# Optimization experiments

Measured on AMD Instinct MI355X. Metric: run time of the kernel, lower is better.

The kernel has to match this reference:

```python
import jax, jax.numpy as jnp
import numpy as np


def setup_inputs() -> dict:
    key = jax.random.key(0)
    ks = jax.random.split(key, 8)
    N, E, H, C, L, G = 100000, 1600000, 128, 10, 5, 64
    x = jax.random.normal(ks[0], (N, H), dtype=jnp.float32)
    edge_index = jax.random.randint(ks[1], (2, E), 0, N, dtype=jnp.int32)
    batch = jnp.sort(jax.random.randint(ks[2], (N,), 0, G, dtype=jnp.int32))
    # Glorot-ish init scale for stability
    Ws = jax.random.normal(ks[3], (L, H, H), dtype=jnp.float32) * (1.0 / np.sqrt(H))
    bs = jax.random.normal(ks[4], (L, H), dtype=jnp.float32) * 0.01
    W_out = jax.random.normal(ks[5], (H, C), dtype=jnp.float32) * (1.0 / np.sqrt(H))
    b_out = jax.random.normal(ks[6], (C,), dtype=jnp.float32) * 0.01
    return {"x": x, "edge_index": edge_index, "batch": batch, "num_graphs": G,
            "Ws": Ws, "bs": bs, "W_out": W_out, "b_out": b_out}


def reference(x, edge_index, batch, num_graphs, Ws, bs, W_out, b_out):
    N = x.shape[0]
    # --- GCN normalization (add self-loops, symmetric deg^-1/2 norm), computed once ---
    loop = jnp.arange(N, dtype=edge_index.dtype)
    src = jnp.concatenate([edge_index[0], loop])  # message sources (x_j)
    dst = jnp.concatenate([edge_index[1], loop])  # aggregation targets
    deg = jax.ops.segment_sum(jnp.ones_like(dst, dtype=x.dtype), dst, num_segments=N)
    dis = jnp.where(deg > 0, jax.lax.rsqrt(jnp.maximum(deg, 1.0)), 0.0)
    norm = dis[src] * dis[dst]  # [E+N]
    # --- stacked GCNConv + ReLU ---
    for l in range(Ws.shape[0]):
        xw = x @ Ws[l]                                   # [N, H] dense transform
        msg = norm[:, None] * xw[src]                    # gather + scale per edge
        x = jax.nn.relu(jax.ops.segment_sum(msg, dst, num_segments=N) + bs[l])
    # --- global mean pool over graphs ---
    sums = jax.ops.segment_sum(x, batch, num_segments=num_graphs)       # [G, H]
    cnts = jax.ops.segment_sum(jnp.ones((N,), x.dtype), batch, num_segments=num_graphs)
    pooled = sums / jnp.maximum(cnts, 1.0)[:, None]
    return pooled @ W_out + b_out
```

## Files before the change

kernel.cpp:

```cpp
#include <hip/hip_runtime.h>
#include <hip/hip_bf16.h>
#include <stdint.h>

#define HDIM 128

typedef __attribute__((ext_vector_type(8))) short short8;
typedef __attribute__((ext_vector_type(4))) float f32x4;

__device__ __forceinline__ ushort f2bf(float f) {
  uint u = __float_as_uint(f);
  u = (u + 0x7fffu + ((u >> 16) & 1u)) >> 16;
  return (ushort)u;
}
__device__ __forceinline__ float bflo(uint v) { return __uint_as_float(v << 16); }
__device__ __forceinline__ float bfhi(uint v) { return __uint_as_float(v & 0xffff0000u); }


__global__ __launch_bounds__(256) void count_kernel(const int* __restrict__ ei,
                                                    int* __restrict__ cnt, int E) {
  int i = blockIdx.x * 256 + threadIdx.x;
  if (i < E) atomicAdd(&cnt[ei[E + i]], 1);
}

__global__ __launch_bounds__(256) void dis_kernel(const int* __restrict__ cnt,
                                                  float* __restrict__ dis, int N) {
  int i = blockIdx.x * 256 + threadIdx.x;
  if (i < N) dis[i] = rsqrtf((float)(cnt[i] + 1));
}

__device__ __forceinline__ int pdeg4(int c) { return (c + 4) & ~3; }

__global__ __launch_bounds__(256) void scan1(const int* __restrict__ cnt,
                                             int* __restrict__ bsum, int N) {
  __shared__ int red[256];
  int b = blockIdx.x, t = threadIdx.x;
  int base = b * 1024;
  int s = 0;
  for (int i = t; i < 1024; i += 256) {
    int n = base + i;
    if (n < N) s += pdeg4(cnt[n]);
  }
  red[t] = s;
  __syncthreads();
  for (int off = 128; off; off >>= 1) {
    if (t < off) red[t] += red[t + off];
    __syncthreads();
  }
  if (t == 0) bsum[b] = red[0];
}

__global__ __launch_bounds__(256) void scan2(int* __restrict__ bsum, int nb) {
  __shared__ int sh[256];
  int t = threadIdx.x;
  int v = (t < nb) ? bsum[t] : 0;
  sh[t] = v;
  __syncthreads();
  for (int off = 1; off < 256; off <<= 1) {
    int add = (t >= off) ? sh[t - off] : 0;
    __syncthreads();
    sh[t] += add;
    __syncthreads();
  }
  if (t < nb) bsum[t] = sh[t] - v;
}

__global__ __launch_bounds__(256) void scan3(const int* __restrict__ cnt,
                                             const int* __restrict__ bsum,
                                             int* __restrict__ rowptr,
                                             int* __restrict__ cursor, int N) {
  __shared__ int sh[256];
  int b = blockIdx.x, t = threadIdx.x;
  int base = b * 1024 + t * 4;
  int v[4];
#pragma unroll
  for (int i = 0; i < 4; ++i) {
    int n = base + i;
    v[i] = (n < N) ? pdeg4(cnt[n]) : 0;
  }
  int tsum = v[0] + v[1] + v[2] + v[3];
  sh[t] = tsum;
  __syncthreads();
  for (int off = 1; off < 256; off <<= 1) {
    int add = (t >= off) ? sh[t - off] : 0;
    __syncthreads();
    sh[t] += add;
    __syncthreads();
  }
  int p = sh[t] - tsum + bsum[b];
#pragma unroll
  for (int i = 0; i < 4; ++i) {
    int n = base + i;
    if (n <= N) rowptr[n] = p;
    if (n < N) cursor[n] = p;
    p += v[i];
  }
}

__device__ __forceinline__ uint pack_cw(int src, float w) {
  uint w15 = (__float_as_uint(w) + 0x8000u) >> 16;
  return (uint)src | (w15 << 17);
}
__device__ __forceinline__ uint cw_src(uint u) { return u & 0x1FFFFu; }
__device__ __forceinline__ float cw_w(uint u) { return __uint_as_float((u >> 17) << 16); }

__global__ __launch_bounds__(256) void fill_csr(const int* __restrict__ ei,
                                                const float* __restrict__ dis,
                                                int* __restrict__ cursor,
                                                uint* __restrict__ colw, int E, int N) {
  int i = blockIdx.x * 256 + threadIdx.x;
  if (i < E) {
    int s = ei[i], d = ei[E + i];
    int pos = atomicAdd(&cursor[d], 1);
    colw[pos] = pack_cw(s, dis[s] * dis[d]);
  } else if (i < E + N) {
    int n = i - E;
    int pos = atomicAdd(&cursor[n], 1);
    colw[pos] = pack_cw(n, dis[n] * dis[n]);
  }
}

__global__ __launch_bounds__(256) void pad_csr(const int* __restrict__ cnt,
                                               const int* __restrict__ rowptr,
                                               uint* __restrict__ colw, int N) {
  int n = blockIdx.x * 256 + threadIdx.x;
  if (n >= N) return;
  int beg = rowptr[n] + cnt[n] + 1, end = rowptr[n + 1];
  for (int j = beg; j < end; ++j) colw[j] = (uint)n;
}

__global__ __launch_bounds__(256) void swz_w(const float* __restrict__ Ws,
                                             ushort* __restrict__ Wsw, int total) {
  int idx = blockIdx.x * 256 + threadIdx.x;
  if (idx >= total) return;
  int l = idx >> 14, r = idx & 16383;
  int j = r & 7, lane = (r >> 3) & 63, kk = (r >> 9) & 3, c = r >> 11;
  int n = c * 16 + (lane & 15);
  int k = kk * 32 + (lane >> 4) * 8 + j;
  Wsw[idx] = f2bf(Ws[l * 16384 + k * HDIM + n]);
}


template <bool F32IN>
__global__ __launch_bounds__(256) void gemm_kernel(const void* __restrict__ Xin,
                                                   const ushort* __restrict__ Wsw,
                                                   ushort* __restrict__ XW, int N,
                                                   int ntiles) {
  __shared__ ushort wlds[16384];
  __shared__ ushort clds[64 * 136];
  const int t = threadIdx.x;
  {
    const int4* src = (const int4*)Wsw;
    int4* dst = (int4*)wlds;
#pragma unroll
    for (int i = 0; i < 8; ++i) dst[t + 256 * i] = src[t + 256 * i];
  }
  __syncthreads();

  const int wave = t >> 6, lane = t & 63;
  const int kq = lane >> 4;

  for (int tile = blockIdx.x; tile < ntiles; tile += gridDim.x) {
    const int row0 = tile * 64 + wave * 16 + (lane & 15);
    const bool inb = row0 < N;

    short8 afr[4];
#pragma unroll
    for (int kk = 0; kk < 4; ++kk) afr[kk] = short8{0, 0, 0, 0, 0, 0, 0, 0};
    if (inb) {
      if constexpr (F32IN) {
        const float* arow = (const float*)Xin + (size_t)row0 * HDIM;
#pragma unroll
        for (int kk = 0; kk < 4; ++kk) {
          float4 x0 = *(const float4*)(arow + kk * 32 + kq * 8);
          float4 x1 = *(const float4*)(arow + kk * 32 + kq * 8 + 4);
          short8 f;
          f[0] = (short)f2bf(x0.x); f[1] = (short)f2bf(x0.y);
          f[2] = (short)f2bf(x0.z); f[3] = (short)f2bf(x0.w);
          f[4] = (short)f2bf(x1.x); f[5] = (short)f2bf(x1.y);
          f[6] = (short)f2bf(x1.z); f[7] = (short)f2bf(x1.w);
          afr[kk] = f;
        }
      } else {
        const short8* arow = (const short8*)((const ushort*)Xin + (size_t)row0 * HDIM);
#pragma unroll
        for (int kk = 0; kk < 4; ++kk) afr[kk] = arow[kk * 4 + kq];
      }
    }

    f32x4 acc[8];
#pragma unroll
    for (int c = 0; c < 8; ++c) acc[c] = f32x4{0.f, 0.f, 0.f, 0.f};
#pragma unroll
    for (int kk = 0; kk < 4; ++kk) {
#pragma unroll
      for (int c = 0; c < 8; ++c) {
        short8 bfr = *(const short8*)(wlds + (((c * 4 + kk) * 64 + lane) << 3));
        acc[c] = __builtin_amdgcn_mfma_f32_16x16x32_bf16(afr[kk], bfr, acc[c], 0, 0, 0);
      }
    }

    __syncthreads();
    const int m0 = wave * 16 + kq * 4;
#pragma unroll
    for (int c = 0; c < 8; ++c) {
      int col = c * 16 + (lane & 15);
#pragma unroll
      for (int r = 0; r < 4; ++r) clds[(m0 + r) * 136 + col] = f2bf(acc[c][r]);
    }
    __syncthreads();
#pragma unroll
    for (int i = 0; i < 4; ++i) {
      int idx = t + 256 * i;
      int row = idx >> 4, piece = idx & 15;
      int grow = tile * 64 + row;
      if (grow < N)
        ((int4*)XW)[(size_t)tile * 1024 + idx] =
            *(const int4*)(clds + row * 136 + piece * 8);
    }
  }
}

__global__ __launch_bounds__(256, 6) void agg_kernel(const ushort* __restrict__ XW,
                                                     const uint* __restrict__ colw,
                                                     const int* __restrict__ rowptr,
                                                     const float* __restrict__ bias,
                                                     ushort* __restrict__ Y, int N) {
  const int lane = threadIdx.x & 63;
  const int node = blockIdx.x * 4 + (threadIdx.x >> 6);
  if (node >= N) return;
  const int e = lane >> 4, c = lane & 15;
  const int beg = rowptr[node];
  const int pdeg = rowptr[node + 1] - beg;
  const int last = pdeg - 1;

  uint cw[6];
#pragma unroll
  for (int k = 0; k < 6; ++k) {
    int off = 4 * k + e;
    cw[k] = __builtin_nontemporal_load(colw + beg + (off < pdeg ? off : last));
  }
  uint4 gv[6];
#pragma unroll
  for (int k = 0; k < 6; ++k)
    gv[k] = *(const uint4*)(XW + ((size_t)cw_src(cw[k]) << 7) + c * 8);

  float acc[8];
#pragma unroll
  for (int i = 0; i < 8; ++i) acc[i] = 0.f;

#pragma unroll
  for (int k = 0; k < 6; ++k) {
    int off = 4 * k + e;
    float w = (off < pdeg) ? cw_w(cw[k]) : 0.f;
    uint4 v = gv[k];
    acc[0] += w * bflo(v.x); acc[1] += w * bfhi(v.x);
    acc[2] += w * bflo(v.y); acc[3] += w * bfhi(v.y);
    acc[4] += w * bflo(v.z); acc[5] += w * bfhi(v.z);
    acc[6] += w * bflo(v.w); acc[7] += w * bfhi(v.w);
  }
  for (int off = 24 + e; off < pdeg; off += 4) {
    uint u = __builtin_nontemporal_load(colw + beg + off);
    uint4 v = *(const uint4*)(XW + ((size_t)cw_src(u) << 7) + c * 8);
    float w = cw_w(u);
    acc[0] += w * bflo(v.x); acc[1] += w * bfhi(v.x);
    acc[2] += w * bflo(v.y); acc[3] += w * bfhi(v.y);
    acc[4] += w * bflo(v.z); acc[5] += w * bfhi(v.z);
    acc[6] += w * bflo(v.w); acc[7] += w * bfhi(v.w);
  }

#pragma unroll
  for (int i = 0; i < 8; ++i) {
    acc[i] += __shfl_xor(acc[i], 16, 64);
    acc[i] += __shfl_xor(acc[i], 32, 64);
  }
  if (e == 0) {
    float4 b0 = *(const float4*)(bias + c * 8);
    float4 b1 = *(const float4*)(bias + c * 8 + 4);
    uint4 pk;
    pk.x = (uint)f2bf(fmaxf(acc[0] + b0.x, 0.f)) | ((uint)f2bf(fmaxf(acc[1] + b0.y, 0.f)) << 16);
    pk.y = (uint)f2bf(fmaxf(acc[2] + b0.z, 0.f)) | ((uint)f2bf(fmaxf(acc[3] + b0.w, 0.f)) << 16);
    pk.z = (uint)f2bf(fmaxf(acc[4] + b1.x, 0.f)) | ((uint)f2bf(fmaxf(acc[5] + b1.y, 0.f)) << 16);
    pk.w = (uint)f2bf(fmaxf(acc[6] + b1.z, 0.f)) | ((uint)f2bf(fmaxf(acc[7] + b1.w, 0.f)) << 16);
    *(uint4*)(Y + (size_t)node * HDIM + c * 8) = pk;
  }
}


__global__ __launch_bounds__(256) void pool_partial(const ushort* __restrict__ x,
                                                    const int* __restrict__ batch,
                                                    float* __restrict__ pooled,
                                                    int* __restrict__ gcnt, int N) {
  const int g = blockIdx.x, s = blockIdx.y;
  const int t = threadIdx.x;
  __shared__ int range[2];
  __shared__ float sums[256];
  if (t < 2) {
    int target = g + t;
    int lo = 0, hi = N;
    while (lo < hi) {
      int mid = (lo + hi) >> 1;
      if (batch[mid] < target) lo = mid + 1;
      else hi = mid;
    }
    range[t] = lo;
  }
  __syncthreads();
  int beg = range[0], end = range[1];
  if (s == 0 && t == 0) gcnt[g] = end - beg;
  int col = t & 127, half = t >> 7;
  float acc = 0.f;
  for (int n = beg + s * 2 + half; n < end; n += 16) {
    acc += __uint_as_float(((uint)x[(size_t)n * HDIM + col]) << 16);
  }
  sums[t] = acc;
  __syncthreads();
  if (t < 128) atomicAdd(&pooled[g * HDIM + t], sums[t] + sums[t + 128]);
}

__global__ __launch_bounds__(256) void out_final(const float* __restrict__ pooled,
                                                 const int* __restrict__ gcnt,
                                                 const float* __restrict__ W_out,
                                                 const float* __restrict__ b_out,
                                                 float* __restrict__ out, int G, int C) {
  int i = blockIdx.x * 256 + threadIdx.x;
  if (i >= G * C) return;
  int g = i / C, c = i - g * C;
  float inv = 1.f / (float)max(gcnt[g], 1);
  const float* pg = pooled + g * HDIM;
  float o = 0.f;
  for (int h = 0; h < HDIM; ++h) o += pg[h] * W_out[h * C + c];
  out[i] = b_out[c] + o * inv;
}


extern "C" void kernel_launch(void* const* d_in, const int* in_sizes, int n_in,
                              void* d_out, int out_size, void* d_ws, size_t ws_size,
                              hipStream_t stream) {
  (void)n_in;
  (void)ws_size;
  const float* x = (const float*)d_in[0];
  const int* ei = (const int*)d_in[1];
  const int* batch = (const int*)d_in[2];
  const float* Ws = (const float*)d_in[4];
  const float* bs = (const float*)d_in[5];
  const float* W_out = (const float*)d_in[6];
  const float* b_out = (const float*)d_in[7];
  float* out = (float*)d_out;

  const int N = in_sizes[0] / HDIM;
  const int E = in_sizes[1] / 2;
  const int L = in_sizes[5] / HDIM;
  const int C = in_sizes[7];
  const int G = out_size / C;

  char* p = (char*)d_ws;
  auto carve = [&](size_t bytes) {
    char* r = p;
    p += (bytes + 255) & ~(size_t)255;
    return r;
  };
  int* cnt = (int*)carve((size_t)N * 4);
  float* dis = (float*)carve((size_t)N * 4);
  int* rowptr = (int*)carve((size_t)(N + 1) * 4);
  int* cursor = (int*)carve((size_t)N * 4);
  int* bsum = (int*)carve(4096);
  uint* colw = (uint*)carve(((size_t)E + 4 * (size_t)N + 64) * 4);
  ushort* Wsw = (ushort*)carve((size_t)L * HDIM * HDIM * 2);
  ushort* xw = (ushort*)carve((size_t)N * HDIM * 2);
  ushort* y0 = (ushort*)carve((size_t)N * HDIM * 2);
  ushort* y1 = (ushort*)carve((size_t)N * HDIM * 2);
  float* pooled = (float*)carve((size_t)G * HDIM * 4 + (size_t)G * 4);
  int* gcnt = (int*)(pooled + (size_t)G * HDIM);

  hipMemsetAsync(cnt, 0, (size_t)N * 4, stream);
  hipMemsetAsync(pooled, 0, (size_t)G * HDIM * 4 + (size_t)G * 4, stream);

  count_kernel<<<(E + 255) / 256, 256, 0, stream>>>(ei, cnt, E);
  dis_kernel<<<(N + 255) / 256, 256, 0, stream>>>(cnt, dis, N);
  int nb = (N + 1 + 1023) / 1024;
  scan1<<<nb, 256, 0, stream>>>(cnt, bsum, N);
  scan2<<<1, 256, 0, stream>>>(bsum, nb);
  scan3<<<nb, 256, 0, stream>>>(cnt, bsum, rowptr, cursor, N);
  fill_csr<<<(E + N + 255) / 256, 256, 0, stream>>>(ei, dis, cursor, colw, E, N);
  pad_csr<<<(N + 255) / 256, 256, 0, stream>>>(cnt, rowptr, colw, N);
  swz_w<<<(L * HDIM * HDIM + 255) / 256, 256, 0, stream>>>(Ws, Wsw, L * HDIM * HDIM);

  const int ntiles = (N + 63) / 64;
  const int gb = 768;
  gemm_kernel<true><<<gb, 256, 0, stream>>>(x, Wsw, xw, N, ntiles);
  agg_kernel<<<(N + 3) / 4, 256, 0, stream>>>(xw, colw, rowptr, bs, y0, N);
  ushort* xc = y0;
  ushort* xn = y1;
  for (int l = 1; l < L; ++l) {
    gemm_kernel<false><<<gb, 256, 0, stream>>>(xc, Wsw + (size_t)l * HDIM * HDIM, xw, N, ntiles);
    agg_kernel<<<(N + 3) / 4, 256, 0, stream>>>(xw, colw, rowptr, bs + (size_t)l * HDIM, xn, N);
    ushort* tmp = xc;
    xc = xn;
    xn = tmp;
  }
  pool_partial<<<dim3(G, 8), 256, 0, stream>>>(xc, batch, pooled, gcnt, N);
  out_final<<<(G * C + 255) / 256, 256, 0, stream>>>(pooled, gcnt, W_out, b_out, out, G, C);
}
```

Baseline: 632.8 us.

## Bucket edges by destination range before CSR fill for locality

The degree-count kernel now also partitions edges into 8 buckets by destination range, and the CSR fill and pad kernels process one bucket per block group (blockIdx & 7). The intent is to keep the scattered atomic cursor updates and colw writes within a narrower address range, improving L2/MALL locality on the multi-XCD GPU. In exchange it adds an extra buffer write and read of all edges, and it relies on a per-bucket capacity of E/4+1024, which could overflow on skewed destination distributions.

Measured after the change: 664.0 us. 1.05x slower.

```diff
diff --git a/kernel.cpp b/kernel.cpp
--- a/kernel.cpp
+++ b/kernel.cpp
@@ -16,10 +16,31 @@
 __device__ __forceinline__ float bfhi(uint v) { return __uint_as_float(v & 0xffff0000u); }
 
 
-__global__ __launch_bounds__(256) void count_kernel(const int* __restrict__ ei,
-                                                    int* __restrict__ cnt, int E) {
-  int i = blockIdx.x * 256 + threadIdx.x;
-  if (i < E) atomicAdd(&cnt[ei[E + i]], 1);
+__global__ __launch_bounds__(256) void bucket_edges(const int* __restrict__ ei,
+                                                    int* __restrict__ cnt,
+                                                    int* __restrict__ bktcur,
+                                                    int2* __restrict__ bkt, int E,
+                                                    float inv8, int cap) {
+  __shared__ int hist[8], base[8];
+  const int t = threadIdx.x;
+  for (int i0 = blockIdx.x * 256; i0 < E; i0 += gridDim.x * 256) {
+    int i = i0 + t;
+    if (t < 8) hist[t] = 0;
+    __syncthreads();
+    int s = 0, d = 0, b = 0, rank = 0;
+    bool valid = i < E;
+    if (valid) {
+      s = ei[i];
+      d = ei[E + i];
+      atomicAdd(&cnt[d], 1);
+      b = min(7, (int)((float)d * inv8));
+      rank = atomicAdd(&hist[b], 1);
+    }
+    __syncthreads();
+    if (t < 8) base[t] = atomicAdd(&bktcur[t], hist[t]);
+    __syncthreads();
+    if (valid) bkt[(size_t)b * cap + base[b] + rank] = make_int2(s, d);
+  }
 }
 
 __global__ __launch_bounds__(256) void dis_kernel(const int* __restrict__ cnt,
@@ -103,29 +124,40 @@
 __device__ __forceinline__ uint cw_src(uint u) { return u & 0x1FFFFu; }
 __device__ __forceinline__ float cw_w(uint u) { return __uint_as_float((u >> 17) << 16); }
 
-__global__ __launch_bounds__(256) void fill_csr(const int* __restrict__ ei,
-                                                const float* __restrict__ dis,
-                                                int* __restrict__ cursor,
-                                                uint* __restrict__ colw, int E, int N) {
-  int i = blockIdx.x * 256 + threadIdx.x;
-  if (i < E) {
-    int s = ei[i], d = ei[E + i];
-    int pos = atomicAdd(&cursor[d], 1);
-    colw[pos] = pack_cw(s, dis[s] * dis[d]);
-  } else if (i < E + N) {
-    int n = i - E;
+__global__ __launch_bounds__(256) void fill_csr2(const int2* __restrict__ bkt,
+                                                 const int* __restrict__ bktcnt,
+                                                 const float* __restrict__ dis,
+                                                 int* __restrict__ cursor,
+                                                 uint* __restrict__ colw, int cap,
+                                                 int E, int N) {
+  const int g = blockIdx.x & 7;
+  const int nb = gridDim.x >> 3;
+  const int bi = blockIdx.x >> 3;
+  const int ecnt = bktcnt[g];
+  const int2* eb = bkt + (size_t)g * cap;
+  for (int i = bi * 256 + threadIdx.x; i < ecnt; i += nb * 256) {
+    int2 sd = eb[i];
+    int pos = atomicAdd(&cursor[sd.y], 1);
+    colw[pos] = pack_cw(sd.x, dis[sd.x] * dis[sd.y]);
+  }
+  const int n0 = (g * N) >> 3, n1 = ((g + 1) * N) >> 3;
+  for (int n = n0 + bi * 256 + threadIdx.x; n < n1; n += nb * 256) {
     int pos = atomicAdd(&cursor[n], 1);
     colw[pos] = pack_cw(n, dis[n] * dis[n]);
   }
 }
 
-__global__ __launch_bounds__(256) void pad_csr(const int* __restrict__ cnt,
-                                               const int* __restrict__ rowptr,
-                                               uint* __restrict__ colw, int N) {
-  int n = blockIdx.x * 256 + threadIdx.x;
-  if (n >= N) return;
-  int beg = rowptr[n] + cnt[n] + 1, end = rowptr[n + 1];
-  for (int j = beg; j < end; ++j) colw[j] = (uint)n;
+__global__ __launch_bounds__(256) void pad_csr2(const int* __restrict__ cnt,
+                                                const int* __restrict__ rowptr,
+                                                uint* __restrict__ colw, int N) {
+  const int g = blockIdx.x & 7;
+  const int nb = gridDim.x >> 3;
+  const int bi = blockIdx.x >> 3;
+  const int n0 = (g * N) >> 3, n1 = ((g + 1) * N) >> 3;
+  for (int n = n0 + bi * 256 + threadIdx.x; n < n1; n += nb * 256) {
+    int beg = rowptr[n] + cnt[n] + 1, end = rowptr[n + 1];
+    for (int j = beg; j < end; ++j) colw[j] = (uint)n;
+  }
 }
 
 __global__ __launch_bounds__(256) void swz_w(const float* __restrict__ Ws,
@@ -352,6 +384,7 @@
   const int L = in_sizes[5] / HDIM;
   const int C = in_sizes[7];
   const int G = out_size / C;
+  const int cap = E / 4 + 1024;
 
   char* p = (char*)d_ws;
   auto carve = [&](size_t bytes) {
@@ -360,10 +393,12 @@
     return r;
   };
   int* cnt = (int*)carve((size_t)N * 4);
+  int* bktcur = (int*)carve(256);
   float* dis = (float*)carve((size_t)N * 4);
   int* rowptr = (int*)carve((size_t)(N + 1) * 4);
   int* cursor = (int*)carve((size_t)N * 4);
   int* bsum = (int*)carve(4096);
+  int2* bkt = (int2*)carve((size_t)8 * cap * 8);
   uint* colw = (uint*)carve(((size_t)E + 4 * (size_t)N + 64) * 4);
   ushort* Wsw = (ushort*)carve((size_t)L * HDIM * HDIM * 2);
   ushort* xw = (ushort*)carve((size_t)N * HDIM * 2);
@@ -373,16 +408,18 @@
   int* gcnt = (int*)(pooled + (size_t)G * HDIM);
 
   hipMemsetAsync(cnt, 0, (size_t)N * 4, stream);
+  hipMemsetAsync(bktcur, 0, 256, stream);
   hipMemsetAsync(pooled, 0, (size_t)G * HDIM * 4 + (size_t)G * 4, stream);
 
-  count_kernel<<<(E + 255) / 256, 256, 0, stream>>>(ei, cnt, E);
+  const float inv8 = 8.0f / (float)N;
+  bucket_edges<<<1024, 256, 0, stream>>>(ei, cnt, bktcur, bkt, E, inv8, cap);
   dis_kernel<<<(N + 255) / 256, 256, 0, stream>>>(cnt, dis, N);
   int nb = (N + 1 + 1023) / 1024;
   scan1<<<nb, 256, 0, stream>>>(cnt, bsum, N);
   scan2<<<1, 256, 0, stream>>>(bsum, nb);
   scan3<<<nb, 256, 0, stream>>>(cnt, bsum, rowptr, cursor, N);
-  fill_csr<<<(E + N + 255) / 256, 256, 0, stream>>>(ei, dis, cursor, colw, E, N);
-  pad_csr<<<(N + 255) / 256, 256, 0, stream>>>(cnt, rowptr, colw, N);
+  fill_csr2<<<1024, 256, 0, stream>>>(bkt, bktcur, dis, cursor, colw, cap, E, N);
+  pad_csr2<<<1024, 256, 0, stream>>>(cnt, rowptr, colw, N);
   swz_w<<<(L * HDIM * HDIM + 255) / 256, 256, 0, stream>>>(Ws, Wsw, L * HDIM * HDIM);
 
   const int ntiles = (N + 63) / 64;
```

## Build CSR via two-level bucket sort with shared-memory histograms

Applied to the files above, without the earlier changes.

Replaces the global-atomic count/scan/fill/pad CSR build with a two-pass scheme. Edges are first binned into 1024-node super-buckets, using block-local histograms and one global atomic per bucket. Per-bucket blocks then count degrees, compute dis, scan, and place edges using shared-memory atomics. This cuts random global atomics and kernel launches, but adds a bucket scratch buffer with a fixed capacity that could overflow on skewed inputs. Only 98 blocks run the counting and placement work, so parallelism in those phases is lower.

Result: faster. 573.5 us (-9.4%).

```diff
diff --git a/kernel.cpp b/kernel.cpp
--- a/kernel.cpp
+++ b/kernel.cpp
@@ -3,6 +3,8 @@
 #include <stdint.h>
 
 #define HDIM 128
+#define SBITS 10
+#define SBMAX 128
 
 typedef __attribute__((ext_vector_type(8))) short short8;
 typedef __attribute__((ext_vector_type(4))) float f32x4;
@@ -15,86 +17,7 @@
 __device__ __forceinline__ float bflo(uint v) { return __uint_as_float(v << 16); }
 __device__ __forceinline__ float bfhi(uint v) { return __uint_as_float(v & 0xffff0000u); }
 
-
-__global__ __launch_bounds__(256) void count_kernel(const int* __restrict__ ei,
-                                                    int* __restrict__ cnt, int E) {
-  int i = blockIdx.x * 256 + threadIdx.x;
-  if (i < E) atomicAdd(&cnt[ei[E + i]], 1);
-}
-
-__global__ __launch_bounds__(256) void dis_kernel(const int* __restrict__ cnt,
-                                                  float* __restrict__ dis, int N) {
-  int i = blockIdx.x * 256 + threadIdx.x;
-  if (i < N) dis[i] = rsqrtf((float)(cnt[i] + 1));
-}
-
 __device__ __forceinline__ int pdeg4(int c) { return (c + 4) & ~3; }
-
-__global__ __launch_bounds__(256) void scan1(const int* __restrict__ cnt,
-                                             int* __restrict__ bsum, int N) {
-  __shared__ int red[256];
-  int b = blockIdx.x, t = threadIdx.x;
-  int base = b * 1024;
-  int s = 0;
-  for (int i = t; i < 1024; i += 256) {
-    int n = base + i;
-    if (n < N) s += pdeg4(cnt[n]);
-  }
-  red[t] = s;
-  __syncthreads();
-  for (int off = 128; off; off >>= 1) {
-    if (t < off) red[t] += red[t + off];
-    __syncthreads();
-  }
-  if (t == 0) bsum[b] = red[0];
-}
-
-__global__ __launch_bounds__(256) void scan2(int* __restrict__ bsum, int nb) {
-  __shared__ int sh[256];
-  int t = threadIdx.x;
-  int v = (t < nb) ? bsum[t] : 0;
-  sh[t] = v;
-  __syncthreads();
-  for (int off = 1; off < 256; off <<= 1) {
-    int add = (t >= off) ? sh[t - off] : 0;
-    __syncthreads();
-    sh[t] += add;
-    __syncthreads();
-  }
-  if (t < nb) bsum[t] = sh[t] - v;
-}
-
-__global__ __launch_bounds__(256) void scan3(const int* __restrict__ cnt,
-                                             const int* __restrict__ bsum,
-                                             int* __restrict__ rowptr,
-                                             int* __restrict__ cursor, int N) {
-  __shared__ int sh[256];
-  int b = blockIdx.x, t = threadIdx.x;
-  int base = b * 1024 + t * 4;
-  int v[4];
-#pragma unroll
-  for (int i = 0; i < 4; ++i) {
-    int n = base + i;
-    v[i] = (n < N) ? pdeg4(cnt[n]) : 0;
-  }
-  int tsum = v[0] + v[1] + v[2] + v[3];
-  sh[t] = tsum;
-  __syncthreads();
-  for (int off = 1; off < 256; off <<= 1) {
-    int add = (t >= off) ? sh[t - off] : 0;
-    __syncthreads();
-    sh[t] += add;
-    __syncthreads();
-  }
-  int p = sh[t] - tsum + bsum[b];
-#pragma unroll
-  for (int i = 0; i < 4; ++i) {
-    int n = base + i;
-    if (n <= N) rowptr[n] = p;
-    if (n < N) cursor[n] = p;
-    p += v[i];
-  }
-}
 
 __device__ __forceinline__ uint pack_cw(int src, float w) {
   uint w15 = (__float_as_uint(w) + 0x8000u) >> 16;
@@ -103,29 +26,151 @@
 __device__ __forceinline__ uint cw_src(uint u) { return u & 0x1FFFFu; }
 __device__ __forceinline__ float cw_w(uint u) { return __uint_as_float((u >> 17) << 16); }
 
-__global__ __launch_bounds__(256) void fill_csr(const int* __restrict__ ei,
-                                                const float* __restrict__ dis,
-                                                int* __restrict__ cursor,
-                                                uint* __restrict__ colw, int E, int N) {
-  int i = blockIdx.x * 256 + threadIdx.x;
-  if (i < E) {
-    int s = ei[i], d = ei[E + i];
-    int pos = atomicAdd(&cursor[d], 1);
-    colw[pos] = pack_cw(s, dis[s] * dis[d]);
-  } else if (i < E + N) {
-    int n = i - E;
-    int pos = atomicAdd(&cursor[n], 1);
-    colw[pos] = pack_cw(n, dis[n] * dis[n]);
-  }
-}
-
-__global__ __launch_bounds__(256) void pad_csr(const int* __restrict__ cnt,
-                                               const int* __restrict__ rowptr,
-                                               uint* __restrict__ colw, int N) {
-  int n = blockIdx.x * 256 + threadIdx.x;
-  if (n >= N) return;
-  int beg = rowptr[n] + cnt[n] + 1, end = rowptr[n + 1];
-  for (int j = beg; j < end; ++j) colw[j] = (uint)n;
+
+__global__ __launch_bounds__(256) void bucket_edges(const int* __restrict__ ei,
+                                                    int* __restrict__ bktcur,
+                                                    uint* __restrict__ bkt, int E,
+                                                    int cap) {
+  __shared__ int hist[SBMAX], base[SBMAX];
+  const int t = threadIdx.x;
+  const int c0 = blockIdx.x * 2048;
+  for (int i = t; i < SBMAX; i += 256) hist[i] = 0;
+  __syncthreads();
+  uint pk[8];
+  int sb_[8], rk[8];
+#pragma unroll
+  for (int j = 0; j < 8; ++j) {
+    int idx = c0 + j * 256 + t;
+    sb_[j] = -1;
+    if (idx < E) {
+      int s = ei[idx];
+      int d = ei[E + idx];
+      int b = d >> SBITS;
+      pk[j] = (uint)(d & 1023) | ((uint)s << SBITS);
+      sb_[j] = b;
+      rk[j] = atomicAdd(&hist[b], 1);
+    }
+  }
+  __syncthreads();
+  for (int i = t; i < SBMAX; i += 256)
+    base[i] = hist[i] ? atomicAdd(&bktcur[i * 16], hist[i]) : 0;
+  __syncthreads();
+#pragma unroll
+  for (int j = 0; j < 8; ++j)
+    if (sb_[j] >= 0)
+      bkt[(size_t)sb_[j] * cap + base[sb_[j]] + rk[j]] = pk[j];
+}
+
+__global__ __launch_bounds__(256) void csr_count(const uint* __restrict__ bkt,
+                                                 const int* __restrict__ bktcur,
+                                                 float* __restrict__ dis,
+                                                 int* __restrict__ sbtot, int cap,
+                                                 int N) {
+  __shared__ int cnt[1024];
+  __shared__ int red[256];
+  const int sb = blockIdx.x, t = threadIdx.x;
+  const int n0 = sb << SBITS;
+  const int ecnt = bktcur[sb * 16];
+  const uint* eb = bkt + (size_t)sb * cap;
+  for (int i = t; i < 1024; i += 256) cnt[i] = 0;
+  __syncthreads();
+  for (int i = t; i < ecnt; i += 256)
+    atomicAdd(&cnt[__builtin_nontemporal_load(eb + i) & 1023], 1);
+  __syncthreads();
+  int s = 0;
+#pragma unroll
+  for (int j = 0; j < 4; ++j) {
+    int idx = t * 4 + j, n = n0 + idx;
+    if (n < N) {
+      dis[n] = rsqrtf((float)(cnt[idx] + 1));
+      s += pdeg4(cnt[idx]);
+    }
+  }
+  red[t] = s;
+  __syncthreads();
+  for (int off = 128; off; off >>= 1) {
+    if (t < off) red[t] += red[t + off];
+    __syncthreads();
+  }
+  if (t == 0) sbtot[sb] = red[0];
+}
+
+__global__ __launch_bounds__(128) void scan_sb(const int* __restrict__ sbtot,
+                                               int* __restrict__ sbbase,
+                                               int* __restrict__ rowptr, int SB,
+                                               int N) {
+  __shared__ int sh[128];
+  int t = threadIdx.x;
+  int v = (t < SB) ? sbtot[t] : 0;
+  sh[t] = v;
+  __syncthreads();
+  for (int off = 1; off < 128; off <<= 1) {
+    int add = (t >= off) ? sh[t - off] : 0;
+    __syncthreads();
+    sh[t] += add;
+    __syncthreads();
+  }
+  if (t < SB) sbbase[t] = sh[t] - v;
+  if (t == 127) rowptr[N] = sh[127];
+}
+
+__global__ __launch_bounds__(256) void csr_place(const uint* __restrict__ bkt,
+                                                 const int* __restrict__ bktcur,
+                                                 const int* __restrict__ sbbase,
+                                                 const float* __restrict__ dis,
+                                                 int* __restrict__ rowptr,
+                                                 uint* __restrict__ colw, int cap,
+                                                 int N) {
+  __shared__ int cnt[1024], cur[1024];
+  __shared__ int sh[256];
+  const int sb = blockIdx.x, t = threadIdx.x;
+  const int n0 = sb << SBITS;
+  const int ecnt = bktcur[sb * 16];
+  const uint* eb = bkt + (size_t)sb * cap;
+  const int base = sbbase[sb];
+  for (int i = t; i < 1024; i += 256) cnt[i] = 0;
+  __syncthreads();
+  for (int i = t; i < ecnt; i += 256)
+    atomicAdd(&cnt[__builtin_nontemporal_load(eb + i) & 1023], 1);
+  __syncthreads();
+  int v[4], tsum = 0;
+#pragma unroll
+  for (int j = 0; j < 4; ++j) {
+    int idx = t * 4 + j, n = n0 + idx;
+    v[j] = (n < N) ? pdeg4(cnt[idx]) : 0;
+    tsum += v[j];
+  }
+  sh[t] = tsum;
+  __syncthreads();
+  for (int off = 1; off < 256; off <<= 1) {
+    int add = (t >= off) ? sh[t - off] : 0;
+    __syncthreads();
+    sh[t] += add;
+    __syncthreads();
+  }
+  int p = sh[t] - tsum;
+#pragma unroll
+  for (int j = 0; j < 4; ++j) {
+    int idx = t * 4 + j, n = n0 + idx;
+    if (n < N) {
+      rowptr[n] = base + p;
+      cur[idx] = p + 1;
+      float dn = dis[n];
+      colw[base + p] = pack_cw(n, dn * dn);
+      int deg = cnt[idx];
+      for (int q = deg + 1; q < v[j]; ++q) colw[base + p + q] = (uint)n;
+    }
+    p += v[j];
+  }
+  __syncthreads();
+  for (int i = t; i < ecnt; i += 256) {
+    uint u = __builtin_nontemporal_load(eb + i);
+    int dloc = (int)(u & 1023);
+    int s2 = (int)(u >> SBITS);
+    int pos = atomicAdd(&cur[dloc], 1);
+    int d = n0 + dloc;
+    colw[base + pos] = pack_cw(s2, dis[s2] * dis[d]);
+  }
 }
 
 __global__ __launch_bounds__(256) void swz_w(const float* __restrict__ Ws,
@@ -352,6 +397,8 @@
   const int L = in_sizes[5] / HDIM;
   const int C = in_sizes[7];
   const int G = out_size / C;
+  const int SB = (N + 1023) >> SBITS;
+  const int cap = E / SB + 8192;
 
   char* p = (char*)d_ws;
   auto carve = [&](size_t bytes) {
@@ -359,11 +406,12 @@
     p += (bytes + 255) & ~(size_t)255;
     return r;
   };
-  int* cnt = (int*)carve((size_t)N * 4);
+  int* bktcur = (int*)carve(SBMAX * 64);
   float* dis = (float*)carve((size_t)N * 4);
   int* rowptr = (int*)carve((size_t)(N + 1) * 4);
-  int* cursor = (int*)carve((size_t)N * 4);
-  int* bsum = (int*)carve(4096);
+  int* sbtot = (int*)carve(SBMAX * 4);
+  int* sbbase = (int*)carve(SBMAX * 4);
+  uint* bkt = (uint*)carve((size_t)SB * cap * 4);
   uint* colw = (uint*)carve(((size_t)E + 4 * (size_t)N + 64) * 4);
   ushort* Wsw = (ushort*)carve((size_t)L * HDIM * HDIM * 2);
   ushort* xw = (ushort*)carve((size_t)N * HDIM * 2);
@@ -372,17 +420,13 @@
   float* pooled = (float*)carve((size_t)G * HDIM * 4 + (size_t)G * 4);
   int* gcnt = (int*)(pooled + (size_t)G * HDIM);
 
-  hipMemsetAsync(cnt, 0, (size_t)N * 4, stream);
+  hipMemsetAsync(bktcur, 0, SBMAX * 64, stream);
   hipMemsetAsync(pooled, 0, (size_t)G * HDIM * 4 + (size_t)G * 4, stream);
 
-  count_kernel<<<(E + 255) / 256, 256, 0, stream>>>(ei, cnt, E);
-  dis_kernel<<<(N + 255) / 256, 256, 0, stream>>>(cnt, dis, N);
-  int nb = (N + 1 + 1023) / 1024;
-  scan1<<<nb, 256, 0, stream>>>(cnt, bsum, N);
-  scan2<<<1, 256, 0, stream>>>(bsum, nb);
-  scan3<<<nb, 256, 0, stream>>>(cnt, bsum, rowptr, cursor, N);
-  fill_csr<<<(E + N + 255) / 256, 256, 0, stream>>>(ei, dis, cursor, colw, E, N);
-  pad_csr<<<(N + 255) / 256, 256, 0, stream>>>(cnt, rowptr, colw, N);
+  bucket_edges<<<(E + 2047) / 2048, 256, 0, stream>>>(ei, bktcur, bkt, E, cap);
+  csr_count<<<SB, 256, 0, stream>>>(bkt, bktcur, dis, sbtot, cap, N);
+  scan_sb<<<1, 128, 0, stream>>>(sbtot, sbbase, rowptr, SB, N);
+  csr_place<<<SB, 256, 0, stream>>>(bkt, bktcur, sbbase, dis, rowptr, colw, cap, N);
   swz_w<<<(L * HDIM * HDIM + 255) / 256, 256, 0, stream>>>(Ws, Wsw, L * HDIM * HDIM);
 
   const int ntiles = (N + 63) / 64;
```
